# Kernel tuning notes

Hardware: AMD Instinct MI355X
Metric: run time of the kernel (lower is better)

Reference implementation:

```python
import jax, jax.numpy as jnp
import numpy as np
from itertools import product

SPATIAL1 = (41, 1600, 1408)  # (z,y,x) = grid[::-1] + [1,0,0]
NUM_BATCH = 2
BN_EPS = 1e-3

# ---------- numpy rulebook construction (spconv-style, done once on host) ----------

def _encode(c, shape):
    D, H, W = [int(v) for v in shape]
    return ((c[:, 0].astype(np.int64) * D + c[:, 1]) * H + c[:, 2]) * W + c[:, 3]

def _lookup(skeys, order, cand):
    pos = np.clip(np.searchsorted(skeys, cand), 0, len(skeys) - 1)
    hit = skeys[pos] == cand
    return hit, order[pos]

def _pad_rb(pairs, n_in, n_out):
    P = max(max(len(a) for a, _ in pairs), 1)
    K = len(pairs)
    ii = np.full((K, P), n_in, np.int32)   # sentinel -> zero feature row
    oo = np.full((K, P), n_out, np.int32)  # sentinel -> dummy output row
    for k, (a, b) in enumerate(pairs):
        ii[k, :len(a)] = a
        oo[k, :len(b)] = b
    return ii, oo

def _subm_rb(coords, shape):
    # SubMConv3d k=3 p=1 s=1: output sites == input sites
    N = len(coords)
    keys = _encode(coords, shape)
    order = np.argsort(keys); skeys = keys[order]
    dims = np.array(shape)
    pairs = []
    for off in product((-1, 0, 1), repeat=3):
        nb = coords[:, 1:] + np.array(off)
        ok = (nb >= 0).all(1) & (nb < dims).all(1)
        oid = np.nonzero(ok)[0]
        cand = _encode(np.concatenate([coords[ok, :1], nb[ok]], 1), shape)
        hit, iid = _lookup(skeys, order, cand)
        pairs.append((iid[hit].astype(np.int32), oid[hit].astype(np.int32)))
    return _pad_rb(pairs, N, N)

def _down_rb(coords, in_shape, ks, st, pd):
    # SparseConv3d: output site active iff any kernel tap hits an active input
    dims = np.array(in_shape); ks = np.array(ks); st = np.array(st); pd = np.array(pd)
    out_shape = (dims + 2 * pd - ks) // st + 1
    offs = list(product(*[range(int(k)) for k in ks]))
    outs = []
    for off in offs:
        o = coords[:, 1:] + pd - np.array(off)
        ok = (o % st == 0).all(1)
        od = o // st
        ok &= (od >= 0).all(1) & (od < out_shape).all(1)
        outs.append(np.concatenate([coords[ok, :1], od[ok]], 1))
    out_coords = np.unique(np.concatenate(outs, 0), axis=0)
    keys = _encode(coords, in_shape)
    order = np.argsort(keys); skeys = keys[order]
    pairs = []
    for off in offs:
        ic = out_coords[:, 1:] * st - pd + np.array(off)
        ok = (ic >= 0).all(1) & (ic < dims).all(1)
        oid = np.nonzero(ok)[0]
        cand = _encode(np.concatenate([out_coords[ok, :1], ic[ok]], 1), in_shape)
        hit, iid = _lookup(skeys, order, cand)
        pairs.append((iid[hit].astype(np.int32), oid[hit].astype(np.int32)))
    ii, oo = _pad_rb(pairs, len(coords), len(out_coords))
    return ii, oo, out_coords, tuple(int(v) for v in out_shape)

def _gen_coords(rng):
    # clustered LiDAR-like active voxels (surfaces -> local density)
    D, H, W = SPATIAL1
    per = []
    for b in range(NUM_BATCH):
        centers = rng.integers([3, 30, 30], [D - 4, H - 31, W - 31], size=(600, 3))
        pts = centers[:, None, :] + rng.integers(-3, 4, size=(600, 60, 3))
        pts = np.clip(pts.reshape(-1, 3), 0, np.array([D - 1, H - 1, W - 1]))
        uniq = np.unique(pts, axis=0)
        per.append(np.concatenate([np.full((len(uniq), 1), b, np.int64), uniq], 1))
    return np.concatenate(per, 0)

CHANS = [(27, 4, 16), (27, 16, 16), (27, 16, 32), (27, 32, 32), (27, 32, 32),
         (27, 32, 64), (27, 64, 64), (27, 64, 64), (27, 64, 64), (27, 64, 64),
         (27, 64, 64), (3, 64, 128)]

def setup_inputs() -> dict:
    rng = np.random.default_rng(0)
    coords = _gen_coords(rng)  # (N,4) [b,z,y,x]
    N = len(coords)
    s1i, s1o = _subm_rb(coords, SPATIAL1)
    d2i, d2o, c2, s2 = _down_rb(coords, SPATIAL1, (3, 3, 3), (2, 2, 2), (1, 1, 1))
    s2i, s2o = _subm_rb(c2, s2)
    d3i, d3o, c3, s3 = _down_rb(c2, s2, (3, 3, 3), (2, 2, 2), (1, 1, 1))
    s3i, s3o = _subm_rb(c3, s3)
    d4i, d4o, c4, s4 = _down_rb(c3, s3, (3, 3, 3), (2, 2, 2), (0, 1, 1))
    s4i, s4o = _subm_rb(c4, s4)
    oi, oo, c5, s5 = _down_rb(c4, s4, (3, 1, 1), (2, 1, 1), (0, 0, 0))

    key = jax.random.key(0)
    ks = jax.random.split(key, 40)
    inp = {}
    for i, (K, ci, co) in enumerate(CHANS):
        inp[f"w{i}"] = (jax.random.normal(ks[i], (K, ci, co), jnp.float32)
                         / np.sqrt(K * ci)).astype(jnp.float32)
        kb = jax.random.split(ks[12 + i], 4)
        inp[f"bn{i}"] = jnp.stack([
            jax.random.uniform(kb[0], (co,)) + 0.5,   # gamma
            jax.random.normal(kb[1], (co,)) * 0.1,    # beta
            jax.random.normal(kb[2], (co,)) * 0.1,    # running mean
            jax.random.uniform(kb[3], (co,)) + 0.5,   # running var
        ]).astype(jnp.float32)
    inp["voxels"] = jax.random.normal(ks[30], (N, 5, 4), jnp.float32)
    inp["voxel_num_points"] = jax.random.randint(ks[31], (N,), 0, 6).astype(jnp.int32)
    for name, arr in [("subm1_in", s1i), ("subm1_out", s1o), ("down2_in", d2i),
                      ("down2_out", d2o), ("subm2_in", s2i), ("subm2_out", s2o),
                      ("down3_in", d3i), ("down3_out", d3o), ("subm3_in", s3i),
                      ("subm3_out", s3o), ("down4_in", d4i), ("down4_out", d4o),
                      ("subm4_in", s4i), ("subm4_out", s4o), ("out_in", oi),
                      ("out_out", oo)]:
        inp[name] = jnp.asarray(arr)
    inp["batch_idx"] = jnp.asarray(c5[:, 0].astype(np.int32))
    inp["n2"] = len(c2); inp["n3"] = len(c3); inp["n4"] = len(c4); inp["n5"] = len(c5)
    inp["n_batch"] = NUM_BATCH
    return inp

# ---------- jax forward ----------

def _sconv(feats, w, in_idx, out_idx, n_out):
    # gather -> per-kernel-offset GEMM -> scatter-add (spconv implicit GEMM)
    fpad = jnp.concatenate([feats, jnp.zeros((1, feats.shape[1]), feats.dtype)], 0)
    g = fpad[in_idx]                                  # (K,P,Cin)
    contrib = jnp.einsum('kpi,kio->kpo', g, w)        # (K,P,Cout)
    out = jnp.zeros((n_out + 1, w.shape[2]), feats.dtype)
    return out.at[out_idx].add(contrib)[:n_out]

def _bnrelu(x, bn):
    g, b, m, v = bn  # eval-mode BatchNorm1d, eps=1e-3
    return jax.nn.relu((x - m) * jax.lax.rsqrt(v + BN_EPS) * g + b)

def reference(voxels, voxel_num_points, w0, w1, w2, w3, w4, w5, w6, w7, w8, w9,
              w10, w11, bn0, bn1, bn2, bn3, bn4, bn5, bn6, bn7, bn8, bn9, bn10,
              bn11, subm1_in, subm1_out, down2_in, down2_out, subm2_in, subm2_out,
              down3_in, down3_out, subm3_in, subm3_out, down4_in, down4_out,
              subm4_in, subm4_out, out_in, out_out, batch_idx, n2, n3, n4, n5,
              n_batch):
    # mean-VFE: average point features per voxel
    denom = jnp.maximum(voxel_num_points.astype(voxels.dtype), 1.0)[:, None]
    x = voxels.sum(1) / denom                              # (N,4)
    n1 = x.shape[0]
    x = _bnrelu(_sconv(x, w0, subm1_in, subm1_out, n1), bn0)   # conv_input
    x = _bnrelu(_sconv(x, w1, subm1_in, subm1_out, n1), bn1)   # conv1
    x = _bnrelu(_sconv(x, w2, down2_in, down2_out, n2), bn2)   # conv2 (s2)
    x = _bnrelu(_sconv(x, w3, subm2_in, subm2_out, n2), bn3)
    x = _bnrelu(_sconv(x, w4, subm2_in, subm2_out, n2), bn4)
    x = _bnrelu(_sconv(x, w5, down3_in, down3_out, n3), bn5)   # conv3 (s2)
    x = _bnrelu(_sconv(x, w6, subm3_in, subm3_out, n3), bn6)
    x = _bnrelu(_sconv(x, w7, subm3_in, subm3_out, n3), bn7)
    x = _bnrelu(_sconv(x, w8, down4_in, down4_out, n4), bn8)   # conv4 (s2)
    x = _bnrelu(_sconv(x, w9, subm4_in, subm4_out, n4), bn9)
    x = _bnrelu(_sconv(x, w10, subm4_in, subm4_out, n4), bn10)
    x = _bnrelu(_sconv(x, w11, out_in, out_out, n5), bn11)     # conv_out
    # dc_feats: per-sample global max pool over active voxels (== max_pool1d)
    dc = jax.ops.segment_max(x, batch_idx, num_segments=n_batch)
    return dc
```

## Files before the change

### kernel.cpp

```cpp
#include <hip/hip_runtime.h>

#define TPB 256
typedef unsigned short u16;
typedef __attribute__((ext_vector_type(8))) short short8v;
typedef __attribute__((ext_vector_type(4))) float f32x4;

__device__ __forceinline__ u16 f2bf(float x) {
    unsigned u = __float_as_uint(x);
    return (u16)((u + 0x7FFFu + ((u >> 16) & 1u)) >> 16);
}
__device__ __forceinline__ float bf2f(u16 h) {
    return __uint_as_float(((unsigned)h) << 16);
}

template<int CS>
__device__ __forceinline__ int swzc(int r, int c) {
    constexpr int PH = (CS == 8) ? 0 : 1;
    return c ^ ((r >> PH) & (CS - 1));
}

__device__ __forceinline__ int xcd_swz(int bid, int nwg) {
    int q = nwg >> 3, r = nwg & 7;
    int x = bid & 7, idx = bid >> 3;
    return (x < r ? x * (q + 1) : r * (q + 1) + (x - r) * q) + idx;
}

__device__ __forceinline__ void gld16(const u16* g, u16* l) {
    __builtin_amdgcn_global_load_lds(
        (const __attribute__((address_space(1))) void*)g,
        (__attribute__((address_space(3))) void*)l, 16, 0, 0);
}

__global__ void vfe_kernel(const float* __restrict__ voxels,
                           const int* __restrict__ nump,
                           float* __restrict__ x, int N) {
    int i = blockIdx.x * blockDim.x + threadIdx.x;
    if (i >= N * 4) return;
    int n = i >> 2, c = i & 3;
    const float* v = voxels + (long)n * 20 + c;
    float s = v[0] + v[4] + v[8] + v[12] + v[16];
    x[i] = s / fmaxf((float)nump[n], 1.0f);
}

struct IBE { const int* rin; const int* rout; int* inv; int P, K, n_in, KP; };
struct IBA { IBE e[8]; };
__global__ void inv_build_all_kernel(IBA a, long grand) {
    long t = (long)blockIdx.x * blockDim.x + threadIdx.x;
    if (t >= grand) return;
    #pragma unroll
    for (int i = 0; i < 8; ++i) {
        if (t < a.e[i].KP) {
            const IBE& E = a.e[i];
            int ii = E.rin[t];
            if (ii != E.n_in) {
                int k = (int)(t / E.P);
                E.inv[(long)E.rout[t] * E.K + k] = ii;
            }
            return;
        }
        t -= a.e[i].KP;
    }
}

struct WPE { const float* w; u16* oh; u16* ol; int K, ci, co, total, paired; };
struct WPA { WPE e[11]; };
__global__ void wprep_kernel(WPA a, long grand) {
    long t = (long)blockIdx.x * blockDim.x + threadIdx.x;
    if (t >= grand) return;
    #pragma unroll
    for (int i = 0; i < 11; ++i) {
        if (t < a.e[i].total) {
            const WPE& E = a.e[i];
            if (E.paired) {
                int p = (int)(t / (E.co * 32));
                int rem = (int)(t % (E.co * 32));
                int o = rem / 32, ci = rem % 32;
                int tap = 2 * p + (ci >> 4);
                float x = (tap < 27) ? E.w[((long)tap * 16 + (ci & 15)) * E.co + o] : 0.f;
                u16 h = f2bf(x);
                float lf = x - bf2f(h);
                int ch = ci >> 3, e = ci & 7;
                int sch = ch ^ ((o >> 1) & 3);
                long d = ((long)p * E.co + o) * 32 + sch * 8 + e;
                E.oh[d] = h; E.ol[d] = f2bf(lf);
            } else {
                int cc = E.ci * E.co;
                int k = (int)(t / cc), r = (int)(t % cc), c = r / E.co, o = r % E.co;
                float x = E.w[t];
                u16 h = f2bf(x);
                float lf = x - bf2f(h);
                int cs = E.ci >> 3, ph = (cs == 8) ? 0 : 1;
                int ch = c >> 3, e = c & 7;
                int sch = ch ^ ((o >> ph) & (cs - 1));
                long d = ((long)k * E.co + o) * E.ci + sch * 8 + e;
                E.oh[d] = h; E.ol[d] = f2bf(lf);
            }
            return;
        }
        t -= a.e[i].total;
    }
}

template<int CO, int K>
__global__ __launch_bounds__(256)
void dconv4_kernel(const float* __restrict__ feats,
                   const float* __restrict__ w,
                   const float* __restrict__ bn,
                   const int* __restrict__ inv,
                   u16* __restrict__ oh, u16* __restrict__ ol,
                   int n_out) {
    constexpr int OG = CO / 4;
    __shared__ float sW[K * 4 * CO];
    for (int i = threadIdx.x; i < K * 4 * CO; i += 256) sW[i] = w[i];
    __syncthreads();
    long t = (long)blockIdx.x * 256 + threadIdx.x;
    int row = (int)(t / OG), og = (int)(t % OG);
    if (row >= n_out) return;
    float a0 = 0.f, a1 = 0.f, a2 = 0.f, a3 = 0.f;
    for (int k = 0; k < K; ++k) {
        int idx = inv[(long)row * K + k];
        if (idx < 0) continue;
        float4 av = *(const float4*)(feats + (long)idx * 4);
        const float* wk = sW + k * 4 * CO + og * 4;
        #pragma unroll
        for (int ci = 0; ci < 4; ++ci) {
            float a = (&av.x)[ci];
            a0 = fmaf(a, wk[ci * CO + 0], a0);
            a1 = fmaf(a, wk[ci * CO + 1], a1);
            a2 = fmaf(a, wk[ci * CO + 2], a2);
            a3 = fmaf(a, wk[ci * CO + 3], a3);
        }
    }
    float4 g = *(const float4*)(bn + og * 4);
    float4 b = *(const float4*)(bn + CO + og * 4);
    float4 m = *(const float4*)(bn + 2 * CO + og * 4);
    float4 v = *(const float4*)(bn + 3 * CO + og * 4);
    float o4[4];
    o4[0] = fmaxf((a0 - m.x) * rsqrtf(v.x + 1e-3f) * g.x + b.x, 0.f);
    o4[1] = fmaxf((a1 - m.y) * rsqrtf(v.y + 1e-3f) * g.y + b.y, 0.f);
    o4[2] = fmaxf((a2 - m.z) * rsqrtf(v.z + 1e-3f) * g.z + b.z, 0.f);
    o4[3] = fmaxf((a3 - m.w) * rsqrtf(v.w + 1e-3f) * g.w + b.w, 0.f);
    long base = (long)row * CO + og * 4;
    #pragma unroll
    for (int c = 0; c < 4; ++c) {
        u16 h = f2bf(o4[c]);
        oh[base + c] = h;
        ol[base + c] = f2bf(o4[c] - bf2f(h));
    }
}

template<int CI, int CO, int ROWS, int KPt, int KT, bool PAIRED, int EPI>
__global__ __launch_bounds__(256, 4)
void mconv_kernel(const u16* __restrict__ fh, const u16* __restrict__ fl,
                  const u16* __restrict__ wh, const u16* __restrict__ wl,
                  const int* __restrict__ inv,
                  const u16* __restrict__ zpage,
                  float* __restrict__ part, long slab_elems,
                  const float* __restrict__ bn,
                  u16* __restrict__ oh, u16* __restrict__ ol,
                  float* __restrict__ outf,
                  int n_out, int kpb) {
    constexpr int CS  = CI / 8;
    constexpr int LCS = (CS == 8) ? 3 : 2;
    constexpr int PH  = (CS == 8) ? 0 : 1;
    constexpr int KS  = CI / 32;
    constexpr int WC  = (ROWS == 128) ? 1 : ((CO >= 32) ? 2 : 1);
    constexpr int WRW = 4 / WC;
    constexpr int MT  = ROWS / (16 * WRW);
    constexpr int NTW = CO / (16 * WC);
    constexpr int ASL = ROWS * CS;
    constexpr int BSL = CO * CS;
    constexpr int AIT = (ASL + 255) / 256;
    constexpr int BIT = (BSL + 255) / 256;

    __shared__ __align__(16) u16 sAh[ROWS * CI];
    __shared__ __align__(16) u16 sAl[ROWS * CI];
    __shared__ __align__(16) u16 sBh[CO * CI];
    __shared__ __align__(16) u16 sBl[CO * CI];

    const int t = threadIdx.x;
    const int bx = xcd_swz(blockIdx.x, gridDim.x);
    const int brow = bx * ROWS;
    const int kbeg = blockIdx.y * kpb;
    const int kend = (kbeg + kpb < KPt) ? (kbeg + kpb) : KPt;

    const int lane = t & 63, wid = t >> 6;
    const int wr = wid / WC, wc = wid % WC;
    const int frow = lane & 15;
    const int fch  = lane >> 4;

    f32x4 acc[MT][NTW];
    #pragma unroll
    for (int mt = 0; mt < MT; ++mt)
        #pragma unroll
        for (int nt = 0; nt < NTW; ++nt) {
            acc[mt][nt][0] = 0.f; acc[mt][nt][1] = 0.f;
            acc[mt][nt][2] = 0.f; acc[mt][nt][3] = 0.f;
        }

    auto stage = [&](int k) {
        #pragma unroll
        for (int s = 0; s < AIT; ++s) {
            int slot = s * 256 + t;
            if (ASL % 256 == 0 || slot < ASL) {
                int r = slot >> LCS, cc = slot & (CS - 1);
                int c = cc ^ ((r >> PH) & (CS - 1));
                int grow = brow + r;
                const u16 *srcH, *srcL;
                if (PAIRED) {
                    int tap = 2 * k + (c >> 1);
                    int idx = (grow < n_out && tap < KT)
                              ? inv[(long)grow * KT + tap] : -1;
                    srcH = (idx >= 0) ? fh + (long)idx * 16 + (c & 1) * 8 : zpage;
                    srcL = (idx >= 0) ? fl + (long)idx * 16 + (c & 1) * 8 : zpage;
                } else {
                    int idx = (grow < n_out) ? inv[(long)grow * KT + k] : -1;
                    srcH = (idx >= 0) ? fh + (long)idx * CI + c * 8 : zpage;
                    srcL = (idx >= 0) ? fl + (long)idx * CI + c * 8 : zpage;
                }
                gld16(srcH, sAh + (s * 256 + wid * 64) * 8);
                gld16(srcL, sAl + (s * 256 + wid * 64) * 8);
            }
        }
        const u16* gbh = wh + (long)k * CO * CI;
        const u16* gbl = wl + (long)k * CO * CI;
        #pragma unroll
        for (int s = 0; s < BIT; ++s) {
            int slot = s * 256 + t;
            if (BSL % 256 == 0 || slot < BSL) {
                gld16(gbh + (long)slot * 8, sBh + (s * 256 + wid * 64) * 8);
                gld16(gbl + (long)slot * 8, sBl + (s * 256 + wid * 64) * 8);
            }
        }
    };
    auto compute = [&]() {
        #pragma unroll
        for (int ks = 0; ks < KS; ++ks) {
            int c = ks * 4 + fch;
            short8v ah[MT], al[MT];
            #pragma unroll
            for (int mt = 0; mt < MT; ++mt) {
                int r = wr * (MT * 16) + mt * 16 + frow;
                int o = r * CI + swzc<CS>(r, c) * 8;
                ah[mt] = *(const short8v*)(sAh + o);
                al[mt] = *(const short8v*)(sAl + o);
            }
            #pragma unroll
            for (int nt = 0; nt < NTW; ++nt) {
                int col = wc * (CO / WC) + nt * 16 + frow;
                int o = col * CI + swzc<CS>(col, c) * 8;
                short8v bh = *(const short8v*)(sBh + o);
                short8v bl = *(const short8v*)(sBl + o);
                #pragma unroll
                for (int mt = 0; mt < MT; ++mt) {
                    acc[mt][nt] = __builtin_amdgcn_mfma_f32_16x16x32_bf16(ah[mt], bh, acc[mt][nt], 0, 0, 0);
                    acc[mt][nt] = __builtin_amdgcn_mfma_f32_16x16x32_bf16(ah[mt], bl, acc[mt][nt], 0, 0, 0);
                    acc[mt][nt] = __builtin_amdgcn_mfma_f32_16x16x32_bf16(al[mt], bh, acc[mt][nt], 0, 0, 0);
                }
            }
        }
    };

    for (int k = kbeg; k < kend; ++k) {
        stage(k);
        __syncthreads();
        compute();
        if (k + 1 < kend) __syncthreads();
    }

    if constexpr (EPI == 0) {
        float* dst = part + (long)blockIdx.y * slab_elems;
        #pragma unroll
        for (int mt = 0; mt < MT; ++mt) {
            int orow0 = brow + wr * (MT * 16) + mt * 16 + (lane >> 4) * 4;
            #pragma unroll
            for (int nt = 0; nt < NTW; ++nt) {
                int ocol = wc * (CO / WC) + nt * 16 + (lane & 15);
                #pragma unroll
                for (int j = 0; j < 4; ++j) {
                    int r = orow0 + j;
                    if (r < n_out) dst[(long)r * CO + ocol] = acc[mt][nt][j];
                }
            }
        }
    } else {
        #pragma unroll
        for (int mt = 0; mt < MT; ++mt) {
            int orow0 = brow + wr * (MT * 16) + mt * 16 + (lane >> 4) * 4;
            #pragma unroll
            for (int nt = 0; nt < NTW; ++nt) {
                int ocol = wc * (CO / WC) + nt * 16 + (lane & 15);
                float g = bn[ocol], bb = bn[CO + ocol];
                float m = bn[2 * CO + ocol], vv = bn[3 * CO + ocol];
                float sc = rsqrtf(vv + 1e-3f) * g;
                #pragma unroll
                for (int j = 0; j < 4; ++j) {
                    int r = orow0 + j;
                    if (r < n_out) {
                        float yv = fmaxf((acc[mt][nt][j] - m) * sc + bb, 0.f);
                        if constexpr (EPI == 1) {
                            u16 h = f2bf(yv);
                            oh[(long)r * CO + ocol] = h;
                            ol[(long)r * CO + ocol] = f2bf(yv - bf2f(h));
                        } else {
                            outf[(long)r * CO + ocol] = yv;
                        }
                    }
                }
            }
        }
    }
}

template<bool EMIT16>
__global__ void reduce_bnrelu_kernel(const float* __restrict__ part, long stride,
                                     int ys, const float* __restrict__ bn, int co,
                                     float* __restrict__ outf,
                                     u16* __restrict__ oh, u16* __restrict__ ol,
                                     long total) {
    long t = (long)blockIdx.x * blockDim.x + threadIdx.x;
    if (t >= total) return;
    float s = 0.f;
    for (int y = 0; y < ys; ++y) s += part[(long)y * stride + t];
    int o = (int)(t % co);
    float g = bn[o], b = bn[co + o], m = bn[2 * co + o], v = bn[3 * co + o];
    float yv = fmaxf((s - m) * rsqrtf(v + 1e-3f) * g + b, 0.f);
    if (EMIT16) {
        u16 h = f2bf(yv);
        oh[t] = h;
        ol[t] = f2bf(yv - bf2f(h));
    } else {
        outf[t] = yv;
    }
}

__global__ void segmax_kernel(const float* __restrict__ x,
                              const int* __restrict__ bidx,
                              float* __restrict__ out, int rows, int nb) {
    __shared__ float sM[8 * 128];
    for (int i = threadIdx.x; i < nb * 128; i += 256) sM[i] = 0.f;
    __syncthreads();
    int c = threadIdx.x & 127;
    int sub = threadIdx.x >> 7;
    for (int r = blockIdx.x * 2 + sub; r < rows; r += gridDim.x * 2) {
        float v = x[(long)r * 128 + c];
        int b = bidx[r];
        atomicMax((int*)&sM[b * 128 + c], __float_as_int(v));
    }
    __syncthreads();
    for (int i = threadIdx.x; i < nb * 128; i += 256)
        atomicMax((int*)out + i, __float_as_int(sM[i]));
}

extern "C" void kernel_launch(void* const* d_in, const int* in_sizes, int n_in,
                              void* d_out, int out_size, void* d_ws, size_t ws_size,
                              hipStream_t stream) {
    (void)n_in;
    const float* voxels = (const float*)d_in[24];
    const int*   nump   = (const int*)d_in[25];
    const int N  = in_sizes[25];
    const int n2 = in_sizes[30] / 27;
    const int n3 = in_sizes[34] / 27;
    const int n4 = in_sizes[38] / 27;
    const int n5 = in_sizes[42];

    struct L { int wi, rb, K, ci, co, nin, nout; };
    const L layers[12] = {
        {0,  26, 27,  4,  16, N,  N }, {1,  26, 27, 16,  16, N,  N },
        {2,  28, 27, 16,  32, N,  n2}, {3,  30, 27, 32,  32, n2, n2},
        {4,  30, 27, 32,  32, n2, n2}, {5,  32, 27, 32,  64, n2, n3},
        {6,  34, 27, 64,  64, n3, n3}, {7,  34, 27, 64,  64, n3, n3},
        {8,  36, 27, 64,  64, n3, n4}, {9,  38, 27, 64,  64, n4, n4},
        {10, 38, 27, 64,  64, n4, n4}, {11, 40,  3, 64, 128, n4, n5},
    };
    struct RBD { int rb, K, nin, nout; };
    const RBD rbs[8] = {
        {26, 27, N,  N }, {28, 27, N,  n2}, {30, 27, n2, n2}, {32, 27, n2, n3},
        {34, 27, n3, n3}, {36, 27, n3, n4}, {38, 27, n4, n4}, {40, 3,  n4, n5},
    };
    const int invmap[12] = {0, 0, 1, 2, 2, 3, 4, 4, 5, 6, 6, 7};
    const int rowsv[12]  = {64, 64, 64, 64, 64, 128, 128, 128, 128, 128, 128, 64};

    size_t feat_elems = (size_t)N * 4, wt_elems = 0, arena_elems = 0;
    for (int i = 0; i < 12; ++i) {
        size_t fe = (size_t)layers[i].nout * layers[i].co;
        if (fe > feat_elems) feat_elems = fe;
        if (i >= 3) wt_elems += (size_t)layers[i].K * layers[i].ci * layers[i].co;
    }
    for (int r = 0; r < 8; ++r) arena_elems += (size_t)rbs[r].nout * rbs[r].K;
    const size_t wp1_elems = 14 * 32 * 16;
    const size_t wp2_elems = 14 * 32 * 32;
    auto al = [](size_t x) { return (x + 255) & ~(size_t)255; };
    char* p = (char*)d_ws;
    u16*   zpage = (u16*)p; p += 256;
    int*   inv_arena = (int*)p; p += al(arena_elems * 4);
    float* bufA = (float*)p; p += al(feat_elems * 4);
    u16* ph[2]; u16* pl[2];
    ph[0] = (u16*)p; p += al(feat_elems * 2);
    pl[0] = (u16*)p; p += al(feat_elems * 2);
    ph[1] = (u16*)p; p += al(feat_elems * 2);
    pl[1] = (u16*)p; p += al(feat_elems * 2);
    u16* wth = (u16*)p; p += al(wt_elems * 2);
    u16* wtl = (u16*)p; p += al(wt_elems * 2);
    u16* wp1h = (u16*)p; p += al(wp1_elems * 2);
    u16* wp1l = (u16*)p; p += al(wp1_elems * 2);
    u16* wp2h = (u16*)p; p += al(wp2_elems * 2);
    u16* wp2l = (u16*)p; p += al(wp2_elems * 2);
    float* slab = (float*)p;
    size_t slab_budget = ws_size - (size_t)((char*)slab - (char*)d_ws);

    hipMemsetAsync(zpage, 0, 256, stream);

    int* invs[8];
    {
        size_t off = 0;
        for (int r = 0; r < 8; ++r) { invs[r] = inv_arena + off; off += (size_t)rbs[r].nout * rbs[r].K; }
        hipMemsetAsync(inv_arena, 0xFF, arena_elems * sizeof(int), stream);
        IBA ia;
        long grand = 0;
        for (int r = 0; r < 8; ++r) {
            int P  = in_sizes[rbs[r].rb] / rbs[r].K;
            ia.e[r].rin  = (const int*)d_in[rbs[r].rb];
            ia.e[r].rout = (const int*)d_in[rbs[r].rb + 1];
            ia.e[r].inv  = invs[r];
            ia.e[r].P = P; ia.e[r].K = rbs[r].K; ia.e[r].n_in = rbs[r].nin;
            ia.e[r].KP = rbs[r].K * P;
            grand += ia.e[r].KP;
        }
        inv_build_all_kernel<<<dim3((unsigned)((grand + TPB - 1) / TPB)), dim3(TPB), 0, stream>>>(ia, grand);
    }

    {
        long tot = (long)N * 4;
        vfe_kernel<<<dim3((unsigned)((tot + TPB - 1) / TPB)), dim3(TPB), 0, stream>>>(
            voxels, nump, bufA, N);
    }

    size_t woff[9];
    {
        WPA wa;
        size_t off = 0;
        for (int i = 0; i < 9; ++i) {
            const L& l = layers[i + 3];
            woff[i] = off;
            wa.e[i].w  = (const float*)d_in[2 * l.wi];
            wa.e[i].oh = wth + off;
            wa.e[i].ol = wtl + off;
            wa.e[i].K = l.K; wa.e[i].ci = l.ci; wa.e[i].co = l.co;
            wa.e[i].total = l.K * l.ci * l.co;
            wa.e[i].paired = 0;
            off += (size_t)wa.e[i].total;
        }
        wa.e[9]  = { (const float*)d_in[2], wp1h, wp1l, 27, 16, 16, (int)wp1_elems, 1 };
        wa.e[10] = { (const float*)d_in[4], wp2h, wp2l, 27, 16, 32, (int)wp2_elems, 1 };
        long grand = (long)off + wp1_elems + wp2_elems;
        wprep_kernel<<<dim3((unsigned)((grand + TPB - 1) / TPB)), dim3(TPB), 0, stream>>>(wa, grand);
    }

    {
        const L& l = layers[0];
        long tot = (long)l.nout * 4;
        dconv4_kernel<16, 27><<<dim3((unsigned)((tot + 255) / 256)), 256, 0, stream>>>(
            bufA, (const float*)d_in[0], (const float*)d_in[1], invs[0],
            ph[0], pl[0], l.nout);
    }

    int cset = 0;
    for (int i = 1; i < 12; ++i) {
        const L& l = layers[i];
        const int* invp = invs[invmap[i]];
        int ROWS = rowsv[i];
        unsigned blocks = (unsigned)((l.nout + ROWS - 1) / ROWS);
        int KPv = (i <= 2) ? 14 : l.K;
        int ysmax = (KPv == 14) ? 9 : ((KPv == 27) ? 27 : 3);
        size_t per = (size_t)l.nout * l.co * 4;
        int ys = 1;
        while (ys < ysmax && blocks * (unsigned)ys < 768) ys *= 3;
        if (ys > ysmax) ys = ysmax;
        while (ys > 1 && (size_t)ys * per > slab_budget) ys /= 3;
        int kpb = (KPv + ys - 1) / ys;
        long slab_elems = (long)l.nout * l.co;
        dim3 grid(blocks, (unsigned)ys);
        const float* bn = (const float*)d_in[2 * l.wi + 1];
        const u16* fh = ph[cset];
        const u16* fl = pl[cset];
        const u16* whp = (i >= 3) ? wth + woff[i - 3] : nullptr;
        const u16* wlp = (i >= 3) ? wtl + woff[i - 3] : nullptr;

        #define MCONV(CI_, CO_, RW_, KP_, KT_, PRD_, WH_, WL_)                         \
            do {                                                                       \
                if (ys == 1 && i < 11)                                                 \
                    mconv_kernel<CI_, CO_, RW_, KP_, KT_, PRD_, 1><<<grid, 256, 0, stream>>>( \
                        fh, fl, WH_, WL_, invp, zpage, nullptr, 0, bn,                 \
                        ph[cset ^ 1], pl[cset ^ 1], nullptr, l.nout, kpb);             \
                else if (ys == 1)                                                      \
                    mconv_kernel<CI_, CO_, RW_, KP_, KT_, PRD_, 2><<<grid, 256, 0, stream>>>( \
                        fh, fl, WH_, WL_, invp, zpage, nullptr, 0, bn,                 \
                        nullptr, nullptr, bufA, l.nout, kpb);                          \
                else                                                                   \
                    mconv_kernel<CI_, CO_, RW_, KP_, KT_, PRD_, 0><<<grid, 256, 0, stream>>>( \
                        fh, fl, WH_, WL_, invp, zpage, slab, slab_elems, bn,           \
                        nullptr, nullptr, nullptr, l.nout, kpb);                       \
            } while (0)

        switch (i) {
        case 1:          MCONV(32, 16, 64, 14, 27, true,  wp1h, wp1l); break;
        case 2:          MCONV(32, 32, 64, 14, 27, true,  wp2h, wp2l); break;
        case 3: case 4:  MCONV(32, 32, 64, 27, 27, false, whp, wlp);   break;
        case 5:          MCONV(32, 64, 128, 27, 27, false, whp, wlp);  break;
        case 11:         MCONV(64, 128, 64, 3, 3,  false, whp, wlp);   break;
        default:         MCONV(64, 64, 128, 27, 27, false, whp, wlp);  break;
        }
        #undef MCONV

        if (ys == 1) {
            if (i < 11) cset ^= 1;
        } else {
            long total = (long)l.nout * l.co;
            unsigned rblocks = (unsigned)((total + TPB - 1) / TPB);
            if (i < 11) {
                reduce_bnrelu_kernel<true><<<dim3(rblocks), dim3(TPB), 0, stream>>>(
                    slab, slab_elems, ys, bn, l.co,
                    nullptr, ph[cset ^ 1], pl[cset ^ 1], total);
                cset ^= 1;
            } else {
                reduce_bnrelu_kernel<false><<<dim3(rblocks), dim3(TPB), 0, stream>>>(
                    slab, slab_elems, ys, bn, l.co, bufA, nullptr, nullptr, total);
            }
        }
    }

    hipMemsetAsync(d_out, 0, (size_t)out_size * sizeof(float), stream);
    const int* bidx = (const int*)d_in[42];
    int nb = out_size / 128;
    segmax_kernel<<<dim3(128), dim3(256), 0, stream>>>(bufA, bidx, (float*)d_out, n5, nb);
}
```

Before: 471.5 us.

## Transpose inverse rulebook to tap-major layout and fix conv tile rows at 64

The inverse rulebook index moves from row-major (row*K+k) to tap-major (k*n_out+row). Consecutive output rows now read contiguous indices for a given tap, which should coalesce the gather-index loads in the staging loop. The ROWS template parameter is also removed, and every mconv layer uses 64-row tiles, including the 64-channel layers that used 128. This raises block count and cuts LDS per block for those layers, at the cost of less weight reuse per block.

Result: faster. 406.4 us (-13.8%).

```diff
diff --git a/kernel.cpp b/kernel.cpp
--- a/kernel.cpp
+++ b/kernel.cpp
@@ -42,7 +42,7 @@
     x[i] = s / fmaxf((float)nump[n], 1.0f);
 }
 
-struct IBE { const int* rin; const int* rout; int* inv; int P, K, n_in, KP; };
+struct IBE { const int* rin; const int* rout; int* inv; int P, K, n_in, n_out, KP; };
 struct IBA { IBE e[8]; };
 __global__ void inv_build_all_kernel(IBA a, long grand) {
     long t = (long)blockIdx.x * blockDim.x + threadIdx.x;
@@ -54,7 +54,7 @@
             int ii = E.rin[t];
             if (ii != E.n_in) {
                 int k = (int)(t / E.P);
-                E.inv[(long)E.rout[t] * E.K + k] = ii;
+                E.inv[(long)k * E.n_out + E.rout[t]] = ii;
             }
             return;
         }
@@ -106,7 +106,7 @@
 void dconv4_kernel(const float* __restrict__ feats,
                    const float* __restrict__ w,
                    const float* __restrict__ bn,
-                   const int* __restrict__ inv,
+                   const int* __restrict__ inv, int inv_n,
                    u16* __restrict__ oh, u16* __restrict__ ol,
                    int n_out) {
     constexpr int OG = CO / 4;
@@ -118,7 +118,7 @@
     if (row >= n_out) return;
     float a0 = 0.f, a1 = 0.f, a2 = 0.f, a3 = 0.f;
     for (int k = 0; k < K; ++k) {
-        int idx = inv[(long)row * K + k];
+        int idx = inv[(long)k * inv_n + row];
         if (idx < 0) continue;
         float4 av = *(const float4*)(feats + (long)idx * 4);
         const float* wk = sW + k * 4 * CO + og * 4;
@@ -149,7 +149,7 @@
     }
 }
 
-template<int CI, int CO, int ROWS, int KPt, int KT, bool PAIRED, int EPI>
+template<int CI, int CO, int KPt, int KT, bool PAIRED, int EPI>
 __global__ __launch_bounds__(256, 4)
 void mconv_kernel(const u16* __restrict__ fh, const u16* __restrict__ fl,
                   const u16* __restrict__ wh, const u16* __restrict__ wl,
@@ -164,23 +164,22 @@
     constexpr int LCS = (CS == 8) ? 3 : 2;
     constexpr int PH  = (CS == 8) ? 0 : 1;
     constexpr int KS  = CI / 32;
-    constexpr int WC  = (ROWS == 128) ? 1 : ((CO >= 32) ? 2 : 1);
-    constexpr int WRW = 4 / WC;
-    constexpr int MT  = ROWS / (16 * WRW);
+    constexpr int WC  = (CO >= 32) ? 2 : 1;
+    constexpr int MT  = (WC == 2) ? 2 : 1;
     constexpr int NTW = CO / (16 * WC);
-    constexpr int ASL = ROWS * CS;
+    constexpr int ASL = 64 * CS;
     constexpr int BSL = CO * CS;
     constexpr int AIT = (ASL + 255) / 256;
     constexpr int BIT = (BSL + 255) / 256;
 
-    __shared__ __align__(16) u16 sAh[ROWS * CI];
-    __shared__ __align__(16) u16 sAl[ROWS * CI];
+    __shared__ __align__(16) u16 sAh[64 * CI];
+    __shared__ __align__(16) u16 sAl[64 * CI];
     __shared__ __align__(16) u16 sBh[CO * CI];
     __shared__ __align__(16) u16 sBl[CO * CI];
 
     const int t = threadIdx.x;
     const int bx = xcd_swz(blockIdx.x, gridDim.x);
-    const int brow = bx * ROWS;
+    const int brow = bx * 64;
     const int kbeg = blockIdx.y * kpb;
     const int kend = (kbeg + kpb < KPt) ? (kbeg + kpb) : KPt;
 
@@ -210,11 +209,11 @@
                 if (PAIRED) {
                     int tap = 2 * k + (c >> 1);
                     int idx = (grow < n_out && tap < KT)
-                              ? inv[(long)grow * KT + tap] : -1;
+                              ? inv[(long)tap * n_out + grow] : -1;
                     srcH = (idx >= 0) ? fh + (long)idx * 16 + (c & 1) * 8 : zpage;
                     srcL = (idx >= 0) ? fl + (long)idx * 16 + (c & 1) * 8 : zpage;
                 } else {
-                    int idx = (grow < n_out) ? inv[(long)grow * KT + k] : -1;
+                    int idx = (grow < n_out) ? inv[(long)k * n_out + grow] : -1;
                     srcH = (idx >= 0) ? fh + (long)idx * CI + c * 8 : zpage;
                     srcL = (idx >= 0) ? fl + (long)idx * CI + c * 8 : zpage;
                 }
@@ -379,7 +378,6 @@
         {34, 27, n3, n3}, {36, 27, n3, n4}, {38, 27, n4, n4}, {40, 3,  n4, n5},
     };
     const int invmap[12] = {0, 0, 1, 2, 2, 3, 4, 4, 5, 6, 6, 7};
-    const int rowsv[12]  = {64, 64, 64, 64, 64, 128, 128, 128, 128, 128, 128, 64};
 
     size_t feat_elems = (size_t)N * 4, wt_elems = 0, arena_elems = 0;
     for (int i = 0; i < 12; ++i) {
@@ -424,6 +422,7 @@
             ia.e[r].rout = (const int*)d_in[rbs[r].rb + 1];
             ia.e[r].inv  = invs[r];
             ia.e[r].P = P; ia.e[r].K = rbs[r].K; ia.e[r].n_in = rbs[r].nin;
+            ia.e[r].n_out = rbs[r].nout;
             ia.e[r].KP = rbs[r].K * P;
             grand += ia.e[r].KP;
         }
@@ -461,7 +460,7 @@
         const L& l = layers[0];
         long tot = (long)l.nout * 4;
         dconv4_kernel<16, 27><<<dim3((unsigned)((tot + 255) / 256)), 256, 0, stream>>>(
-            bufA, (const float*)d_in[0], (const float*)d_in[1], invs[0],
+            bufA, (const float*)d_in[0], (const float*)d_in[1], invs[0], l.nout,
             ph[0], pl[0], l.nout);
     }
 
@@ -469,8 +468,7 @@
     for (int i = 1; i < 12; ++i) {
         const L& l = layers[i];
         const int* invp = invs[invmap[i]];
-        int ROWS = rowsv[i];
-        unsigned blocks = (unsigned)((l.nout + ROWS - 1) / ROWS);
+        unsigned blocks = (unsigned)((l.nout + 63) / 64);
         int KPv = (i <= 2) ? 14 : l.K;
         int ysmax = (KPv == 14) ? 9 : ((KPv == 27) ? 27 : 3);
         size_t per = (size_t)l.nout * l.co * 4;
@@ -487,29 +485,29 @@
         const u16* whp = (i >= 3) ? wth + woff[i - 3] : nullptr;
         const u16* wlp = (i >= 3) ? wtl + woff[i - 3] : nullptr;
 
-        #define MCONV(CI_, CO_, RW_, KP_, KT_, PRD_, WH_, WL_)                         \
+        #define MCONV(CI_, CO_, KP_, KT_, PRD_, WH_, WL_)                              \
             do {                                                                       \
                 if (ys == 1 && i < 11)                                                 \
-                    mconv_kernel<CI_, CO_, RW_, KP_, KT_, PRD_, 1><<<grid, 256, 0, stream>>>( \
+                    mconv_kernel<CI_, CO_, KP_, KT_, PRD_, 1><<<grid, 256, 0, stream>>>( \
                         fh, fl, WH_, WL_, invp, zpage, nullptr, 0, bn,                 \
                         ph[cset ^ 1], pl[cset ^ 1], nullptr, l.nout, kpb);             \
                 else if (ys == 1)                                                      \
-                    mconv_kernel<CI_, CO_, RW_, KP_, KT_, PRD_, 2><<<grid, 256, 0, stream>>>( \
+                    mconv_kernel<CI_, CO_, KP_, KT_, PRD_, 2><<<grid, 256, 0, stream>>>( \
                         fh, fl, WH_, WL_, invp, zpage, nullptr, 0, bn,                 \
                         nullptr, nullptr, bufA, l.nout, kpb);                          \
                 else                                                                   \
-                    mconv_kernel<CI_, CO_, RW_, KP_, KT_, PRD_, 0><<<grid, 256, 0, stream>>>( \
+                    mconv_kernel<CI_, CO_, KP_, KT_, PRD_, 0><<<grid, 256, 0, stream>>>( \
                         fh, fl, WH_, WL_, invp, zpage, slab, slab_elems, bn,           \
                         nullptr, nullptr, nullptr, l.nout, kpb);                       \
             } while (0)
 
         switch (i) {
-        case 1:          MCONV(32, 16, 64, 14, 27, true,  wp1h, wp1l); break;
-        case 2:          MCONV(32, 32, 64, 14, 27, true,  wp2h, wp2l); break;
-        case 3: case 4:  MCONV(32, 32, 64, 27, 27, false, whp, wlp);   break;
-        case 5:          MCONV(32, 64, 128, 27, 27, false, whp, wlp);  break;
-        case 11:         MCONV(64, 128, 64, 3, 3,  false, whp, wlp);   break;
-        default:         MCONV(64, 64, 128, 27, 27, false, whp, wlp);  break;
+        case 1:          MCONV(32, 16, 14, 27, true,  wp1h, wp1l); break;
+        case 2:          MCONV(32, 32, 14, 27, true,  wp2h, wp2l); break;
+        case 3: case 4:  MCONV(32, 32, 27, 27, false, whp, wlp);   break;
+        case 5:          MCONV(32, 64, 27, 27, false, whp, wlp);   break;
+        case 11:         MCONV(64, 128, 3, 3,  false, whp, wlp);   break;
+        default:         MCONV(64, 64, 27, 27, false, whp, wlp);   break;
         }
         #undef MCONV
 
```
